# Kernel tuning notes

Measured on AMD Instinct MI355X. Metric: run time of the kernel, lower is better.

## Reference

```python
import jax, jax.numpy as jnp
import numpy as np

N, R, D, T, H, MM, OBJ, PLN = 1024, 100, 256, 14, 8, 600, 36, 16
DH = D // H


def _plin(w, x):
    # monotone piecewise-linear map on [0,1] with PLN segments (Counter's PiecewiseLin)
    w = jnp.abs(w).at[0].set(0.0)
    w = w / w.sum()
    cs = jnp.cumsum(w)  # knot values, cs[PLN] == 1
    y = PLN * jnp.clip(x, 0.0, 1.0)
    i = jnp.clip(jnp.floor(y).astype(jnp.int32), 0, PLN)
    f = y - jnp.floor(y)
    return cs[i] + f * w[jnp.clip(i + 1, 0, PLN)]


def _iou(b):
    # b: (N, m, 4) as x1,y1,x2,y2 -> pairwise IoU (N, m, m)
    area = jnp.clip(b[..., 2] - b[..., 0], 0.0) * jnp.clip(b[..., 3] - b[..., 1], 0.0)
    lt = jnp.maximum(b[:, :, None, :2], b[:, None, :, :2])
    rb = jnp.minimum(b[:, :, None, 2:], b[:, None, :, 2:])
    wh = jnp.clip(rb - lt, 0.0)
    inter = wh[..., 0] * wh[..., 1]
    return inter / (area[:, :, None] + area[:, None, :] - inter + 1e-12)


def _counter(boxes, att, pw):
    # Zhang et al. counting module, already_sigmoided=True
    att_top, idx = jax.lax.top_k(att, OBJ)                       # (N, m)
    btop = jnp.take_along_axis(boxes, idx[:, :, None], axis=1)   # (N, m, 4)
    rel = att_top[:, :, None] * att_top[:, None, :]              # outer product of attention
    dist = 1.0 - _iou(btop)
    score = _plin(pw[0], rel) * _plin(pw[1], dist)
    dscore = _plin(pw[3], rel) * _plin(pw[4], dist)
    # deduplication via outer differences
    att_diff = jnp.abs(att_top[:, :, None] - att_top[:, None, :])
    sd = jnp.abs(dscore[:, :, :, None] - dscore[:, :, None, :])  # (N, m, m, m)
    sim = jnp.prod(_plin(pw[2], 1.0 - sd), axis=1) * _plin(pw[2], 1.0 - att_diff)
    row_sims = sim.sum(axis=2)                                   # (N, m), >= 1 (diagonal)
    all_sims = row_sims[:, :, None] * row_sims[:, None, :]
    score = score / all_sims
    correction = _plin(pw[0], att_top * att_top) / row_sims
    total = jnp.sqrt(score.sum(axis=(1, 2)) + correction.sum(axis=1) + 1e-20)  # (N,)
    # to_one_hot: soft one-hot between floor and ceil counts
    s = jnp.clip(total, 0.0, float(OBJ))
    i = jnp.clip(jnp.floor(s).astype(jnp.int32), 0, OBJ)
    f = s - jnp.floor(s)
    oh_l = jax.nn.one_hot(i, OBJ + 1, dtype=s.dtype)
    oh_r = jax.nn.one_hot(jnp.clip(i + 1, 0, OBJ), OBJ + 1, dtype=s.dtype)
    one_hot = (1.0 - f)[:, None] * oh_l + f[:, None] * oh_r
    att_conf = jnp.abs(_plin(pw[5], att_top) - 0.5)
    dist_conf = jnp.abs(_plin(pw[6], dist) - 0.5)
    conf = _plin(pw[7], att_conf.mean(axis=1) + dist_conf.mean(axis=(1, 2)))  # (N,)
    return one_hot * conf[:, None], conf


def _layernorm(x, g, b):
    mu = x.mean(-1, keepdims=True)
    var = ((x - mu) ** 2).mean(-1, keepdims=True)
    return (x - mu) / jnp.sqrt(var + 1e-5) * g + b


def setup_inputs():
    key = jax.random.key(0)
    ks = jax.random.split(key, 20)
    lin = lambda k, o, i: jax.random.normal(k, (o, i), dtype=jnp.float32) * 0.02
    z = lambda o: jnp.zeros((o,), jnp.float32)
    v_emb = jax.random.normal(ks[0], (N, R, D), dtype=jnp.float32)
    q_emb = jax.random.normal(ks[1], (N, T, D), dtype=jnp.float32)
    xy = jax.random.uniform(ks[2], (N, R, 2), dtype=jnp.float32) * 0.8
    wh = jax.random.uniform(ks[3], (N, R, 2), dtype=jnp.float32) * 0.19 + 0.01
    boxes = jnp.concatenate([xy, xy + wh], axis=-1)  # valid x1,y1,x2,y2 in [0,1]
    pw = jax.random.uniform(ks[4], (8, PLN + 1), dtype=jnp.float32, minval=0.5, maxval=1.5)
    pw = pw.at[:, 0].set(0.0)
    return {
        'v_emb': v_emb, 'q_emb': q_emb, 'boxes': boxes,
        'Wq': lin(ks[5], D, D), 'bq': z(D),
        'Wk': lin(ks[6], D, D), 'bk': z(D),
        'Wv': lin(ks[7], D, D), 'bv': z(D),
        'in_w': lin(ks[8], 3 * D, D), 'in_b': z(3 * D),
        'out_w': lin(ks[9], D, D), 'out_b': z(D),
        'ln_g': jnp.ones((D,), jnp.float32), 'ln_b': z(D),
        'l0_w': lin(ks[10], MM, D), 'l0_b': z(MM),
        'l1_w': lin(ks[11], MM, D), 'l1_b': z(MM),
        'lo_w': lin(ks[12], 1, MM), 'lo_b': z(1),
        'pw': pw,
    }


def reference(v_emb, q_emb, boxes, Wq, bq, Wk, bk, Wv, bv, in_w, in_b, out_w, out_b,
              ln_g, ln_b, l0_w, l0_b, l1_w, l1_b, lo_w, lo_b, pw):
    n = v_emb.shape[0]
    # pre-projections then nn.MultiheadAttention (eval, no dropout)
    q = v_emb @ Wq.T + bq
    k = v_emb @ Wk.T + bk
    v = v_emb @ Wv.T + bv
    wq, wk, wv = jnp.split(in_w, 3, axis=0)
    biq, bik, biv = jnp.split(in_b, 3)
    qh = (q @ wq.T + biq).reshape(n, R, H, DH)
    kh = (k @ wk.T + bik).reshape(n, R, H, DH)
    vh = (v @ wv.T + biv).reshape(n, R, H, DH)
    logits = jnp.einsum('nqhd,nkhd->nhqk', qh, kh) * (1.0 / np.sqrt(DH))
    attn = jax.nn.softmax(logits, axis=-1)
    ao = jnp.einsum('nhqk,nkhd->nqhd', attn, vh).reshape(n, R, D)
    ao = ao @ out_w.T + out_b
    inter = _layernorm(ao, ln_g, ln_b)
    # MLB bilinear fusion with mean-pooled question, normalize=True, no activations
    q_pool = q_emb.mean(axis=1)                 # (N, D)
    x0 = inter @ l0_w.T + l0_b                  # (N, R, MM)
    x1 = q_pool @ l1_w.T + l1_b                 # (N, MM)
    zf = x0 * x1[:, None, :]
    zf = jnp.sign(zf) * jnp.sqrt(jnp.abs(zf))   # signed sqrt
    zf = zf / jnp.maximum(jnp.linalg.norm(zf, axis=-1, keepdims=True), 1e-12)
    scores = jax.nn.sigmoid(zf @ lo_w.T + lo_b)  # (N, R, 1)
    pred, conf = _counter(boxes, scores[..., 0], pw)
    return scores, pred, conf
```

## Files before the change

kernel.cpp:

```cpp
#include <hip/hip_runtime.h>

#define N_   1024
#define R_   100
#define D_   256
#define T_   14
#define H_   8
#define DH_  32
#define MM_  600
#define OBJ_ 36

typedef _Float16 f16;
typedef __attribute__((ext_vector_type(8))) _Float16 f16x8;
typedef __attribute__((ext_vector_type(4))) _Float16 f16x4v;
typedef __attribute__((ext_vector_type(4))) float f32x4;

__device__ __forceinline__ void f2h_split(float x, f16& hi, f16& lo) {
  hi = (_Float16)x;
  lo = (_Float16)(x - (float)hi);
}

#define GL16(gp, lp) __builtin_amdgcn_global_load_lds( \
    (const __attribute__((address_space(1))) void*)(gp), \
    (__attribute__((address_space(3))) void*)(lp), 16, 0, 0)

__device__ __forceinline__ void xcd_remap(int& bx, int& by) {
  int nx = gridDim.x, ny = gridDim.y;
  if ((nx & 7) == 0) {
    int id = bx + nx * by;
    int xcd = id & 7, slot = id >> 3;
    bx = xcd + 8 * (slot / ny);
    by = slot % ny;
  }
}

__device__ __forceinline__ float plin_f(const float* __restrict__ w,
                                        const float* __restrict__ cs, float x) {
  float xc = fminf(fmaxf(x, 0.f), 1.f);
  float y  = 16.f * xc;
  float fy = floorf(y);
  int   i  = (int)fy;
  float f  = y - fy;
  int   ip = i + 1; if (ip > 16) ip = 16;
  return cs[i] + f * w[ip];
}

__global__ void prep_plin(const float* __restrict__ pw, float* __restrict__ plw,
                          float* __restrict__ plc) {
  int p = threadIdx.x;
  if (p < 8) {
    float w[17];
    float sum = 0.f;
    w[0] = 0.f;
    for (int k = 1; k < 17; ++k) { w[k] = fabsf(pw[p*17 + k]); sum += w[k]; }
    float inv = 1.f / sum;
    float c = 0.f;
    for (int k = 0; k < 17; ++k) {
      float wk = w[k] * inv;
      c += wk;
      plw[p*17 + k] = wk;
      plc[p*17 + k] = c;
    }
  }
}

__global__ void fuse_c(const float* __restrict__ in_w, const float* __restrict__ in_b,
                       const float* __restrict__ bq, const float* __restrict__ bk,
                       const float* __restrict__ bv, float* __restrict__ c) {
  int i = blockIdx.x * blockDim.x + threadIdx.x;
  if (i < 768) {
    const float* bsel = (i < 256) ? bq : ((i < 512) ? bk : bv);
    float acc = in_b[i];
    for (int o = 0; o < 256; ++o) acc += in_w[(size_t)i*256 + o] * bsel[o];
    c[i] = acc;
  }
}

__global__ __launch_bounds__(256) void fuse_A(const float* __restrict__ in_w,
    const float* __restrict__ Wq, const float* __restrict__ Wk,
    const float* __restrict__ Wv, f16* __restrict__ Ahi, f16* __restrict__ Alo) {
  int i = blockIdx.x;
  int j = threadIdx.x;
  const float* Wsel = (i < 256) ? Wq : ((i < 512) ? Wk : Wv);
  __shared__ float row[256];
  row[j] = in_w[(size_t)i*256 + j];
  __syncthreads();
  float acc = 0.f;
  for (int o = 0; o < 256; ++o) acc += row[o] * Wsel[(size_t)o*256 + j];
  f16 h, l; f2h_split(acc, h, l);
  Ahi[(size_t)i*256 + j] = h;
  Alo[(size_t)i*256 + j] = l;
}

__global__ __launch_bounds__(256) void split_vec(const float* __restrict__ in,
    f16* __restrict__ hi, f16* __restrict__ lo, int n4) {
  int i = blockIdx.x * blockDim.x + threadIdx.x;
  if (i < n4) {
    float4 v = ((const float4*)in)[i];
    union { f16 h[4]; ushort4 u; } H, L;
    f2h_split(v.x, H.h[0], L.h[0]);
    f2h_split(v.y, H.h[1], L.h[1]);
    f2h_split(v.z, H.h[2], L.h[2]);
    f2h_split(v.w, H.h[3], L.h[3]);
    ((ushort4*)hi)[i] = H.u;
    ((ushort4*)lo)[i] = L.u;
  }
}

__global__ __launch_bounds__(256) void conv_w600(const float* __restrict__ w,
    f16* __restrict__ hi, f16* __restrict__ lo) {
  int o = blockIdx.x;
  int j = threadIdx.x;
  f16 h = (f16)0.f, l = (f16)0.f;
  if (o < 600) f2h_split(w[(size_t)o*256 + j], h, l);
  hi[(size_t)o*256 + j] = h;
  lo[(size_t)o*256 + j] = l;
}

__global__ __launch_bounds__(256) void pool_split(const float* __restrict__ q_emb,
    f16* __restrict__ qph, f16* __restrict__ qpl) {
  int n = blockIdx.x, tid = threadIdx.x;
  float s = 0.f;
  for (int t = 0; t < 14; ++t) s += q_emb[((size_t)n*14 + t)*256 + tid];
  s *= (1.f/14.f);
  f16 h, l; f2h_split(s, h, l);
  qph[(size_t)n*256 + tid] = h;
  qpl[(size_t)n*256 + tid] = l;
}

template<bool BOUND>
__global__ __launch_bounds__(256) void gemm_f16s(
    const f16* __restrict__ Xhi, const f16* __restrict__ Xlo,
    const f16* __restrict__ Whi, const f16* __restrict__ Wlo,
    const float* __restrict__ bias, float* __restrict__ C, int Oreal) {
  __shared__ f16 XsH[128 * 32];
  __shared__ f16 XsL[128 * 32];
  __shared__ f16 WsH[128 * 32];
  __shared__ f16 WsL[128 * 32];
  const int tid  = threadIdx.x;
  const int wave = tid >> 6, lane = tid & 63;
  int bx = blockIdx.x, by = blockIdx.y;
  xcd_remap(bx, by);
  const int bm = bx * 128, bn = by * 128;
  const int wm = (wave & 1) * 64, wn = (wave >> 1) * 64;
  const int col = lane & 15, quad = lane >> 4;

  const int s = wave * 64 + lane;
  const int r0 = s >> 2,         cseg = (s & 3) * 8;
  const int r1 = (s + 256) >> 2;
  const size_t o0 = (size_t)(bm + r0) * 256 + cseg;
  const size_t o1 = (size_t)(bm + r1) * 256 + cseg;
  const size_t p0 = (size_t)(bn + r0) * 256 + cseg;
  const size_t p1 = (size_t)(bn + r1) * 256 + cseg;
  char* XHB = (char*)XsH + wave * 1024;
  char* XLB = (char*)XsL + wave * 1024;
  char* WHB = (char*)WsH + wave * 1024;
  char* WLB = (char*)WsL + wave * 1024;

  f32x4 acc[4][4] = {};

  for (int k0 = 0; k0 < 256; k0 += 32) {
    GL16(Xhi + o0 + k0, XHB);
    GL16(Xhi + o1 + k0, XHB + 4096);
    GL16(Xlo + o0 + k0, XLB);
    GL16(Xlo + o1 + k0, XLB + 4096);
    GL16(Whi + p0 + k0, WHB);
    GL16(Whi + p1 + k0, WHB + 4096);
    GL16(Wlo + p0 + k0, WLB);
    GL16(Wlo + p1 + k0, WLB + 4096);
    __syncthreads();

    f16x8 ah[4], al[4], bh[4], bl[4];
#pragma unroll
    for (int i = 0; i < 4; ++i) {
      int ro = (wm + i*16 + col) * 32 + quad * 8;
      ah[i] = *(const f16x8*)(XsH + ro);
      al[i] = *(const f16x8*)(XsL + ro);
    }
#pragma unroll
    for (int j = 0; j < 4; ++j) {
      int ro = (wn + j*16 + col) * 32 + quad * 8;
      bh[j] = *(const f16x8*)(WsH + ro);
      bl[j] = *(const f16x8*)(WsL + ro);
    }
#pragma unroll
    for (int i = 0; i < 4; ++i)
#pragma unroll
      for (int j = 0; j < 4; ++j) {
        acc[i][j] = __builtin_amdgcn_mfma_f32_16x16x32_f16(al[i], bh[j], acc[i][j], 0, 0, 0);
        acc[i][j] = __builtin_amdgcn_mfma_f32_16x16x32_f16(ah[i], bl[j], acc[i][j], 0, 0, 0);
        acc[i][j] = __builtin_amdgcn_mfma_f32_16x16x32_f16(ah[i], bh[j], acc[i][j], 0, 0, 0);
      }
    __syncthreads();
  }

#pragma unroll
  for (int j = 0; j < 4; ++j) {
    int o = bn + wn + j*16 + col;
    if (BOUND && o >= Oreal) continue;
    float bo = bias[o];
#pragma unroll
    for (int i = 0; i < 4; ++i) {
#pragma unroll
      for (int r = 0; r < 4; ++r) {
        int m = bm + wm + i*16 + quad*4 + r;
        C[(size_t)m * Oreal + o] = acc[i][j][r] + bo;
      }
    }
  }
}

__global__ __launch_bounds__(256) void gemm_l0_mlb(
    const f16* __restrict__ Xhi, const f16* __restrict__ Xlo,
    const f16* __restrict__ Whi, const f16* __restrict__ Wlo,
    const float* __restrict__ bias, const float* __restrict__ x1,
    const float* __restrict__ lo_w, float2* __restrict__ part) {
  __shared__ f16 XsH[128 * 32];
  __shared__ f16 XsL[128 * 32];
  __shared__ f16 WsH[128 * 32];
  __shared__ f16 WsL[128 * 32];
  const int tid  = threadIdx.x;
  const int wave = tid >> 6, lane = tid & 63;
  int bx = blockIdx.x, by = blockIdx.y;
  xcd_remap(bx, by);
  const int bm = bx * 128, bn = by * 128;
  const int wm = (wave & 1) * 64, wn = (wave >> 1) * 64;
  const int col = lane & 15, quad = lane >> 4;

  const int s = wave * 64 + lane;
  const int r0 = s >> 2,         cseg = (s & 3) * 8;
  const int r1 = (s + 256) >> 2;
  const size_t o0 = (size_t)(bm + r0) * 256 + cseg;
  const size_t o1 = (size_t)(bm + r1) * 256 + cseg;
  const size_t p0 = (size_t)(bn + r0) * 256 + cseg;
  const size_t p1 = (size_t)(bn + r1) * 256 + cseg;
  char* XHB = (char*)XsH + wave * 1024;
  char* XLB = (char*)XsL + wave * 1024;
  char* WHB = (char*)WsH + wave * 1024;
  char* WLB = (char*)WsL + wave * 1024;

  f32x4 acc[4][4] = {};

  for (int k0 = 0; k0 < 256; k0 += 32) {
    GL16(Xhi + o0 + k0, XHB);
    GL16(Xhi + o1 + k0, XHB + 4096);
    GL16(Xlo + o0 + k0, XLB);
    GL16(Xlo + o1 + k0, XLB + 4096);
    GL16(Whi + p0 + k0, WHB);
    GL16(Whi + p1 + k0, WHB + 4096);
    GL16(Wlo + p0 + k0, WLB);
    GL16(Wlo + p1 + k0, WLB + 4096);
    __syncthreads();

    f16x8 ah[4], al[4], bh[4], bl[4];
#pragma unroll
    for (int i = 0; i < 4; ++i) {
      int ro = (wm + i*16 + col) * 32 + quad * 8;
      ah[i] = *(const f16x8*)(XsH + ro);
      al[i] = *(const f16x8*)(XsL + ro);
    }
#pragma unroll
    for (int j = 0; j < 4; ++j) {
      int ro = (wn + j*16 + col) * 32 + quad * 8;
      bh[j] = *(const f16x8*)(WsH + ro);
      bl[j] = *(const f16x8*)(WsL + ro);
    }
#pragma unroll
    for (int i = 0; i < 4; ++i)
#pragma unroll
      for (int j = 0; j < 4; ++j) {
        acc[i][j] = __builtin_amdgcn_mfma_f32_16x16x32_f16(al[i], bh[j], acc[i][j], 0, 0, 0);
        acc[i][j] = __builtin_amdgcn_mfma_f32_16x16x32_f16(ah[i], bl[j], acc[i][j], 0, 0, 0);
        acc[i][j] = __builtin_amdgcn_mfma_f32_16x16x32_f16(ah[i], bh[j], acc[i][j], 0, 0, 0);
      }
    __syncthreads();
  }

  const int M = (int)gridDim.x * 128;
  const int NCimg = M / 100;
  const int mA = bm + wm;
  const int imgA = mA / 100;
  int imgB = imgA + 1; if (imgB > NCimg - 1) imgB = NCimg - 1;
  const int rB = (imgA + 1) * 100;

  float bo4[4], lw4[4], x1A[4], x1B[4];
#pragma unroll
  for (int j = 0; j < 4; ++j) {
    int o = bn + wn + j*16 + col;
    bool v = (o < 600);
    bo4[j] = v ? bias[o] : 0.f;
    lw4[j] = v ? lo_w[o] : 0.f;
    x1A[j] = v ? x1[(size_t)imgA*600 + o] : 0.f;
    x1B[j] = v ? x1[(size_t)imgB*600 + o] : 0.f;
  }

#pragma unroll
  for (int i = 0; i < 4; ++i) {
#pragma unroll
    for (int rr = 0; rr < 4; ++rr) {
      int m = bm + wm + i*16 + quad*4 + rr;
      bool hiImg = (m >= rB);
      float ss = 0.f, dt = 0.f;
#pragma unroll
      for (int j = 0; j < 4; ++j) {
        float xv = hiImg ? x1B[j] : x1A[j];
        float v = (acc[i][j][rr] + bo4[j]) * xv;
        float av = fabsf(v);
        ss += av;
        dt += copysignf(sqrtf(av), v) * lw4[j];
      }
#pragma unroll
      for (int msk = 1; msk < 16; msk <<= 1) {
        ss += __shfl_xor(ss, msk, 64);
        dt += __shfl_xor(dt, msk, 64);
      }
      if (col == 0) {
        float2 pv; pv.x = ss; pv.y = dt;
        part[(size_t)m * 10 + by * 2 + (wn >> 6)] = pv;
      }
    }
  }
}

__global__ __launch_bounds__(256) void mlb_reduce(const float2* __restrict__ part,
    const float* __restrict__ lo_b, float* __restrict__ out, int M) {
  int m = blockIdx.x * 256 + threadIdx.x;
  if (m < M) {
    const float2* p = part + (size_t)m * 10;
    float ss = 0.f, dt = 0.f;
#pragma unroll
    for (int t = 0; t < 10; ++t) { float2 v = p[t]; ss += v.x; dt += v.y; }
    float sc = dt / fmaxf(sqrtf(ss), 1e-12f) + lo_b[0];
    out[m] = 1.f / (1.f + __expf(-sc));
  }
}

__global__ __launch_bounds__(256) void gemm2_ln(
    const f16* __restrict__ Xhi, const f16* __restrict__ Xlo,
    const f16* __restrict__ Whi, const f16* __restrict__ Wlo,
    const float* __restrict__ bias, const float* __restrict__ g,
    const float* __restrict__ b, f16* __restrict__ ohi, f16* __restrict__ olo) {
  __shared__ f16 XsH[128 * 32];
  __shared__ f16 XsL[128 * 32];
  __shared__ f16 WsH[256 * 32];
  __shared__ f16 WsL[256 * 32];
  __shared__ float gbb[768];
  const int tid  = threadIdx.x;
  const int wave = tid >> 6, lane = tid & 63;
  const int bm = blockIdx.x * 128;
  const int wm = wave * 32;
  const int col16 = lane & 15, quad = lane >> 4;

  for (int i = tid; i < 768; i += 256)
    gbb[i] = (i < 256) ? g[i] : ((i < 512) ? b[i - 256] : bias[i - 512]);

  const int s = wave * 64 + lane;
  const int rx0 = s >> 2, cseg = (s & 3) * 8;
  const int rx1 = (s + 256) >> 2;
  const size_t o0 = (size_t)(bm + rx0) * 256 + cseg;
  const size_t o1 = (size_t)(bm + rx1) * 256 + cseg;
  char* XHB = (char*)XsH + wave * 1024;
  char* XLB = (char*)XsL + wave * 1024;

  f32x4 acc[2][16] = {};

  for (int k0 = 0; k0 < 256; k0 += 32) {
    GL16(Xhi + o0 + k0, XHB);
    GL16(Xhi + o1 + k0, XHB + 4096);
    GL16(Xlo + o0 + k0, XLB);
    GL16(Xlo + o1 + k0, XLB + 4096);
#pragma unroll
    for (int is = 0; is < 4; ++is) {
      int sw = is * 256 + s;
      size_t wo = (size_t)(sw >> 2) * 256 + (sw & 3) * 8 + k0;
      GL16(Whi + wo, (char*)WsH + is * 4096 + wave * 1024);
      GL16(Wlo + wo, (char*)WsL + is * 4096 + wave * 1024);
    }
    __syncthreads();

    f16x8 ah[2], al[2];
#pragma unroll
    for (int i = 0; i < 2; ++i) {
      int ro = (wm + i*16 + col16) * 32 + quad * 8;
      ah[i] = *(const f16x8*)(XsH + ro);
      al[i] = *(const f16x8*)(XsL + ro);
    }
#pragma unroll
    for (int j = 0; j < 16; ++j) {
      int ro = (j*16 + col16) * 32 + quad * 8;
      f16x8 bh = *(const f16x8*)(WsH + ro);
      f16x8 bl = *(const f16x8*)(WsL + ro);
#pragma unroll
      for (int i = 0; i < 2; ++i) {
        acc[i][j] = __builtin_amdgcn_mfma_f32_16x16x32_f16(al[i], bh, acc[i][j], 0, 0, 0);
        acc[i][j] = __builtin_amdgcn_mfma_f32_16x16x32_f16(ah[i], bl, acc[i][j], 0, 0, 0);
        acc[i][j] = __builtin_amdgcn_mfma_f32_16x16x32_f16(ah[i], bh, acc[i][j], 0, 0, 0);
      }
    }
    __syncthreads();
  }

#pragma unroll
  for (int i = 0; i < 2; ++i) {
#pragma unroll
    for (int r = 0; r < 4; ++r) {
      float x[16];
      float sum = 0.f;
#pragma unroll
      for (int j = 0; j < 16; ++j) {
        float v = acc[i][j][r] + gbb[512 + j*16 + col16];
        x[j] = v;
        sum += v;
      }
#pragma unroll
      for (int msk = 1; msk < 16; msk <<= 1) sum += __shfl_xor(sum, msk, 64);
      float mu = sum * (1.f/256.f);
      float s2 = 0.f;
#pragma unroll
      for (int j = 0; j < 16; ++j) { float d = x[j] - mu; s2 += d * d; }
#pragma unroll
      for (int msk = 1; msk < 16; msk <<= 1) s2 += __shfl_xor(s2, msk, 64);
      float inv = rsqrtf(s2 * (1.f/256.f) + 1e-5f);
      size_t m = (size_t)(bm + wm + i*16 + quad*4 + r);
#pragma unroll
      for (int j = 0; j < 16; ++j) {
        int col = j*16 + col16;
        float yv = (x[j] - mu) * inv * gbb[col] + gbb[256 + col];
        f16 hh, ll; f2h_split(yv, hh, ll);
        ohi[m*256 + col] = hh;
        olo[m*256 + col] = ll;
      }
    }
  }
}

__global__ __launch_bounds__(512) void attn_mfma(const float* __restrict__ qkv,
    f16* __restrict__ aohi, f16* __restrict__ aolo) {
  const int n = blockIdx.x >> 3;
  const int h = blockIdx.x & 7;
  __shared__ f16 KH[112*32], KL[112*32];
  __shared__ f16 VTH[32*116], VTL[32*116];
  __shared__ unsigned int P32[112*116];
  const int tid = threadIdx.x;
  const int wave = tid >> 6, lane = tid & 63;
  const int col16 = lane & 15, quad = lane >> 4;
  const float scale = 0.17677669529663687f;
  const float* base = qkv + (size_t)n * 100 * 768 + h * 32;
  const int tm = wave;

  float qv[8];
  if (tm < 7) {
    int m = tm*16 + col16; if (m > 99) m = 99;
    const float* qp = base + (size_t)m * 768 + quad*8;
    float4 q0 = *(const float4*)(qp);
    float4 q1 = *(const float4*)(qp + 4);
    qv[0]=q0.x; qv[1]=q0.y; qv[2]=q0.z; qv[3]=q0.w;
    qv[4]=q1.x; qv[5]=q1.y; qv[6]=q1.z; qv[7]=q1.w;
  } else {
#pragma unroll
    for (int j = 0; j < 8; ++j) qv[j] = 0.f;
  }

  for (int idx = tid; idx < 112*32; idx += 512) {
    int r = idx >> 5, d = idx & 31;
    float kv = 0.f, vv = 0.f;
    if (r < 100) {
      const float* p = base + (size_t)r * 768;
      kv = p[256 + d];
      vv = p[512 + d];
    }
    f16 khh, kll, vhh, vll;
    f2h_split(kv, khh, kll);
    f2h_split(vv, vhh, vll);
    KH[idx] = khh; KL[idx] = kll;
    VTH[d*116 + r] = vhh; VTL[d*116 + r] = vll;
  }
  __syncthreads();

  if (tm < 7) {
    f16x8 ah, al;
#pragma unroll
    for (int j = 0; j < 8; ++j) {
      f16 hh, ll; f2h_split(qv[j] * scale, hh, ll); ah[j] = hh; al[j] = ll;
    }
    f32x4 sacc[7];
#pragma unroll
    for (int tn = 0; tn < 7; ++tn) {
      int off = (tn*16 + col16)*32 + quad*8;
      f16x8 bh = *(const f16x8*)(KH + off);
      f16x8 bl = *(const f16x8*)(KL + off);
      f32x4 a = {};
      a = __builtin_amdgcn_mfma_f32_16x16x32_f16(al, bh, a, 0, 0, 0);
      a = __builtin_amdgcn_mfma_f32_16x16x32_f16(ah, bl, a, 0, 0, 0);
      a = __builtin_amdgcn_mfma_f32_16x16x32_f16(ah, bh, a, 0, 0, 0);
      sacc[tn] = a;
    }
    if (col16 >= 4) {
      sacc[6][0] = -1e30f; sacc[6][1] = -1e30f;
      sacc[6][2] = -1e30f; sacc[6][3] = -1e30f;
    }
    float mx[4];
#pragma unroll
    for (int r = 0; r < 4; ++r) {
      float mv = sacc[0][r];
#pragma unroll
      for (int tn = 1; tn < 7; ++tn) mv = fmaxf(mv, sacc[tn][r]);
      mx[r] = mv;
    }
#pragma unroll
    for (int msk = 1; msk < 16; msk <<= 1)
#pragma unroll
      for (int r = 0; r < 4; ++r) mx[r] = fmaxf(mx[r], __shfl_xor(mx[r], msk, 64));
    float sm[4] = {0.f, 0.f, 0.f, 0.f};
#pragma unroll
    for (int tn = 0; tn < 7; ++tn)
#pragma unroll
      for (int r = 0; r < 4; ++r) {
        float p = __expf(sacc[tn][r] - mx[r]);
        sacc[tn][r] = p;
        sm[r] += p;
      }
#pragma unroll
    for (int msk = 1; msk < 16; msk <<= 1)
#pragma unroll
      for (int r = 0; r < 4; ++r) sm[r] += __shfl_xor(sm[r], msk, 64);
    float inv[4];
#pragma unroll
    for (int r = 0; r < 4; ++r) inv[r] = 1.f / sm[r];
#pragma unroll
    for (int tn = 0; tn < 7; ++tn)
#pragma unroll
      for (int r = 0; r < 4; ++r) {
        float p = sacc[tn][r] * inv[r];
        f16 hh, ll; f2h_split(p, hh, ll);
        union { struct { f16 h, l; } f; unsigned int u; } pk;
        pk.f.h = hh; pk.f.l = ll;
        P32[(tm*16 + quad*4 + r)*116 + tn*16 + col16] = pk.u;
      }

    f16x8 vh[2][4], vl[2][4];
#pragma unroll
    for (int td = 0; td < 2; ++td)
#pragma unroll
      for (int kc = 0; kc < 4; ++kc) {
        if (kc == 3 && quad >= 2) {
          f16x8 z = {};
          vh[td][kc] = z; vl[td][kc] = z;
        } else {
          int off = (td*16 + col16)*116 + kc*32 + quad*8;
          f16x4v h0 = *(const f16x4v*)(VTH + off);
          f16x4v h1 = *(const f16x4v*)(VTH + off + 4);
          f16x4v l0 = *(const f16x4v*)(VTL + off);
          f16x4v l1 = *(const f16x4v*)(VTL + off + 4);
          f16x8 hv, lv;
#pragma unroll
          for (int t = 0; t < 4; ++t) { hv[t] = h0[t]; hv[t+4] = h1[t]; lv[t] = l0[t]; lv[t+4] = l1[t]; }
          vh[td][kc] = hv; vl[td][kc] = lv;
        }
      }
    f32x4 acc[2] = {};
#pragma unroll
    for (int kc = 0; kc < 4; ++kc) {
      f16x8 ph, pl;
      if (kc == 3 && quad >= 2) {
        f16x8 z = {};
        ph = z; pl = z;
      } else {
        const unsigned int* pp = P32 + (tm*16 + col16)*116 + kc*32 + quad*8;
        f16x8 e0 = *(const f16x8*)(pp);
        f16x8 e1 = *(const f16x8*)(pp + 4);
        ph = __builtin_shufflevector(e0, e1, 0, 2, 4, 6, 8, 10, 12, 14);
        pl = __builtin_shufflevector(e0, e1, 1, 3, 5, 7, 9, 11, 13, 15);
      }
#pragma unroll
      for (int td = 0; td < 2; ++td) {
        acc[td] = __builtin_amdgcn_mfma_f32_16x16x32_f16(pl, vh[td][kc], acc[td], 0, 0, 0);
        acc[td] = __builtin_amdgcn_mfma_f32_16x16x32_f16(ph, vl[td][kc], acc[td], 0, 0, 0);
        acc[td] = __builtin_amdgcn_mfma_f32_16x16x32_f16(ph, vh[td][kc], acc[td], 0, 0, 0);
      }
    }
#pragma unroll
    for (int td = 0; td < 2; ++td) {
#pragma unroll
      for (int r = 0; r < 4; ++r) {
        int m = tm*16 + quad*4 + r;
        if (m < 100) {
          size_t oidx = ((size_t)n*100 + m)*256 + h*32 + td*16 + col16;
          f16 hh, ll; f2h_split(acc[td][r], hh, ll);
          aohi[oidx] = hh;
          aolo[oidx] = ll;
        }
      }
    }
  }
}

__device__ __forceinline__ float breduce(float v, float* red, int tid) {
  for (int o = 32; o > 0; o >>= 1) v += __shfl_down(v, o, 64);
  if ((tid & 63) == 0) red[tid >> 6] = v;
  __syncthreads();
  float r = red[0] + red[1] + red[2] + red[3];
  __syncthreads();
  return r;
}

__global__ __launch_bounds__(256) void counter_kernel(
    const float* __restrict__ scores, const float* __restrict__ boxes,
    const float* __restrict__ plw, const float* __restrict__ plc,
    float* __restrict__ pred, float* __restrict__ conf_out) {
  int n = blockIdx.x, tid = threadIdx.x;
  __shared__ float plw_s[8][17], plc_s[8][17];
  __shared__ float sval[128];
  __shared__ int   sidx[128];
  __shared__ float att[36], bx[36][4];
  __shared__ float dist[36][36], scr[36][36], ds2[36][36], sim[36][36];
  __shared__ float rs[36];
  __shared__ float red[4];
  __shared__ float b_f, b_cf;
  __shared__ int   b_i;

  for (int i = tid; i < 136; i += 256) {
    (&plw_s[0][0])[i] = plw[i];
    (&plc_s[0][0])[i] = plc[i];
  }
  if (tid < 128) {
    sval[tid] = (tid < 100) ? scores[(size_t)n*100 + tid] : -1e30f;
    sidx[tid] = tid;
  }
  __syncthreads();

  for (int k = 2; k <= 128; k <<= 1) {
    for (int j = k >> 1; j > 0; j >>= 1) {
      if (tid < 128) {
        int ixj = tid ^ j;
        if (ixj > tid) {
          float va = sval[tid], vb = sval[ixj];
          int   ia = sidx[tid], ib = sidx[ixj];
          bool a_before_b = (va > vb) || (va == vb && ia < ib);
          bool ascending = ((tid & k) == 0);
          bool doswap = ascending ? !a_before_b : a_before_b;
          if (doswap) { sval[tid] = vb; sval[ixj] = va; sidx[tid] = ib; sidx[ixj] = ia; }
        }
      }
      __syncthreads();
    }
  }

  if (tid < 36) {
    att[tid] = sval[tid];
    const float* bp = boxes + ((size_t)n*100 + sidx[tid])*4;
    bx[tid][0] = bp[0]; bx[tid][1] = bp[1]; bx[tid][2] = bp[2]; bx[tid][3] = bp[3];
  }
  __syncthreads();

  for (int idx = tid; idx < 1296; idx += 256) {
    int i = idx / 36, j = idx % 36;
    float x1a = bx[i][0], y1a = bx[i][1], x2a = bx[i][2], y2a = bx[i][3];
    float x1b = bx[j][0], y1b = bx[j][1], x2b = bx[j][2], y2b = bx[j][3];
    float areaA = fmaxf(x2a - x1a, 0.f) * fmaxf(y2a - y1a, 0.f);
    float areaB = fmaxf(x2b - x1b, 0.f) * fmaxf(y2b - y1b, 0.f);
    float iw = fmaxf(fminf(x2a, x2b) - fmaxf(x1a, x1b), 0.f);
    float ih = fmaxf(fminf(y2a, y2b) - fmaxf(y1a, y1b), 0.f);
    float inter = iw * ih;
    float iou = inter / (areaA + areaB - inter + 1e-12f);
    float dd = 1.f - iou;
    float rel = att[i] * att[j];
    dist[i][j] = dd;
    scr[i][j]  = plin_f(plw_s[0], plc_s[0], rel) * plin_f(plw_s[1], plc_s[1], dd);
    ds2[i][j]  = plin_f(plw_s[3], plc_s[3], rel) * plin_f(plw_s[4], plc_s[4], dd);
  }
  __syncthreads();

  for (int idx = tid; idx < 1296; idx += 256) {
    int b = idx / 36, c = idx % 36;
    float p = plin_f(plw_s[2], plc_s[2], 1.f - fabsf(att[b] - att[c]));
    for (int a = 0; a < 36; ++a)
      p *= plin_f(plw_s[2], plc_s[2], 1.f - fabsf(ds2[a][b] - ds2[a][c]));
    sim[b][c] = p;
  }
  __syncthreads();

  if (tid < 36) {
    float s = 0.f;
    for (int c = 0; c < 36; ++c) s += sim[tid][c];
    rs[tid] = s;
  }
  __syncthreads();

  float p1 = 0.f, p4 = 0.f;
  for (int idx = tid; idx < 1296; idx += 256) {
    int b = idx / 36, c = idx % 36;
    p1 += scr[b][c] / (rs[b] * rs[c]);
    p4 += fabsf(plin_f(plw_s[6], plc_s[6], dist[b][c]) - 0.5f);
  }
  float p2 = 0.f, p3 = 0.f;
  if (tid < 36) {
    p2 = plin_f(plw_s[0], plc_s[0], att[tid]*att[tid]) / rs[tid];
    p3 = fabsf(plin_f(plw_s[5], plc_s[5], att[tid]) - 0.5f);
  }
  float s1 = breduce(p1, red, tid);
  float s2 = breduce(p2, red, tid);
  float s3 = breduce(p3, red, tid);
  float s4 = breduce(p4, red, tid);

  if (tid == 0) {
    float total = sqrtf(s1 + s2 + 1e-20f);
    float cf = plin_f(plw_s[7], plc_s[7], s3 * (1.f/36.f) + s4 * (1.f/1296.f));
    float sc = fminf(fmaxf(total, 0.f), 36.f);
    float fl = floorf(sc);
    int ii = (int)fl; if (ii > 36) ii = 36;
    b_f = sc - fl;
    b_i = ii;
    b_cf = cf;
    conf_out[n] = cf;
  }
  __syncthreads();
  if (tid < 37) {
    int ii = b_i;
    int ir = (ii + 1 > 36) ? 36 : ii + 1;
    float v = ((tid == ii) ? (1.f - b_f) : 0.f) + ((tid == ir) ? b_f : 0.f);
    pred[(size_t)n*37 + tid] = v * b_cf;
  }
}

extern "C" void kernel_launch(void* const* d_in, const int* in_sizes, int n_in,
                              void* d_out, int out_size, void* d_ws, size_t ws_size,
                              hipStream_t stream) {
  const float* v_emb = (const float*)d_in[0];
  const float* q_emb = (const float*)d_in[1];
  const float* boxes = (const float*)d_in[2];
  const float* Wq    = (const float*)d_in[3];
  const float* bq    = (const float*)d_in[4];
  const float* Wk    = (const float*)d_in[5];
  const float* bk    = (const float*)d_in[6];
  const float* Wv    = (const float*)d_in[7];
  const float* bv    = (const float*)d_in[8];
  const float* in_w  = (const float*)d_in[9];
  const float* in_b  = (const float*)d_in[10];
  const float* out_w = (const float*)d_in[11];
  const float* out_b = (const float*)d_in[12];
  const float* ln_g  = (const float*)d_in[13];
  const float* ln_b  = (const float*)d_in[14];
  const float* l0_w  = (const float*)d_in[15];
  const float* l0_b  = (const float*)d_in[16];
  const float* l1_w  = (const float*)d_in[17];
  const float* l1_b  = (const float*)d_in[18];
  const float* lo_w  = (const float*)d_in[19];
  const float* lo_b  = (const float*)d_in[20];
  const float* pw    = (const float*)d_in[21];

  float* ws = (float*)d_ws;
  float* plw   = ws + 0;
  float* plc   = ws + 256;
  float* cbuf  = ws + 512;
  float* x1    = ws + 1280;
  f16* hb = (f16*)(ws + 615680);
  f16* A_hi    = hb + 0;
  f16* A_lo    = hb + 196608;
  f16* outw_hi = hb + 393216;
  f16* outw_lo = hb + 458752;
  f16* l0w_hi  = hb + 524288;
  f16* l0w_lo  = hb + 688128;
  f16* l1w_hi  = hb + 851968;
  f16* l1w_lo  = hb + 1015808;
  f16* qp_hi   = hb + 1179648;
  f16* qp_lo   = hb + 1441792;
  f16* v_hi    = hb + 1703936;
  f16* v_lo    = hb + 27918336;
  const size_t small_floats = 615680 + 27066368;

  size_t avail = (ws_size / 4 > small_floats) ? (ws_size / 4 - small_floats) : 0;
  int NC = 1024;
  while (NC > 32 && (size_t)NC * 130000ull > avail) NC >>= 1;

  float* qkv_c = ws + small_floats;
  float2* part = (float2*)(qkv_c + (size_t)NC * 76800);
  f16* ao_hi  = (f16*)((float*)(void*)part + (size_t)NC * 2000);
  f16* ao_lo  = ao_hi + (size_t)NC * 25600;
  f16* int_hi = ao_lo + (size_t)NC * 25600;
  f16* int_lo = int_hi + (size_t)NC * 25600;

  float* out    = (float*)d_out;
  float* scores = out;
  float* pred   = out + 102400;
  float* conf   = out + 140288;

  prep_plin<<<1, 64, 0, stream>>>(pw, plw, plc);
  fuse_c<<<3, 256, 0, stream>>>(in_w, in_b, bq, bk, bv, cbuf);
  fuse_A<<<768, 256, 0, stream>>>(in_w, Wq, Wk, Wv, A_hi, A_lo);
  split_vec<<<(65536/4 + 255)/256, 256, 0, stream>>>(out_w, outw_hi, outw_lo, 65536/4);
  conv_w600<<<640, 256, 0, stream>>>(l0_w, l0w_hi, l0w_lo);
  conv_w600<<<640, 256, 0, stream>>>(l1_w, l1w_hi, l1w_lo);
  split_vec<<<(26214400/4 + 255)/256, 256, 0, stream>>>(v_emb, v_hi, v_lo, 26214400/4);
  pool_split<<<N_, 256, 0, stream>>>(q_emb, qp_hi, qp_lo);
  {
    dim3 gx(1024/128, 5);
    gemm_f16s<true><<<gx, 256, 0, stream>>>(qp_hi, qp_lo, l1w_hi, l1w_lo,
                                            l1_b, x1, 600);
  }

  for (int n0 = 0; n0 < N_; n0 += NC) {
    const int M = NC * 100;
    const size_t voff = (size_t)n0 * 100 * 256;

    dim3 g1(M / 128, 6);
    gemm_f16s<false><<<g1, 256, 0, stream>>>(v_hi + voff, v_lo + voff,
                                             A_hi, A_lo, cbuf, qkv_c, 768);

    attn_mfma<<<NC * H_, 512, 0, stream>>>(qkv_c, ao_hi, ao_lo);

    gemm2_ln<<<M / 128, 256, 0, stream>>>(ao_hi, ao_lo, outw_hi, outw_lo,
                                          out_b, ln_g, ln_b, int_hi, int_lo);

    dim3 g3(M / 128, 5);
    gemm_l0_mlb<<<g3, 256, 0, stream>>>(int_hi, int_lo, l0w_hi, l0w_lo,
                                        l0_b, x1 + (size_t)n0 * 600, lo_w, part);

    mlb_reduce<<<(M + 255)/256, 256, 0, stream>>>(part, lo_b,
                                                  scores + (size_t)n0 * 100, M);
  }

  counter_kernel<<<N_, 256, 0, stream>>>(scores, boxes, plw, plc, pred, conf);
}
```

Before: 882.0 us.

## Fuse QKV projection GEMM into per-head attention kernel

Removes the separate QKV GEMM and its fp32 intermediate buffer. Each attention block now computes its own head's Q, K and V projections from the split-f16 v_emb and the fused weight matrix, staging tiles into LDS with global_load_lds. The results go straight into the K/V LDS layouts and a swizzled Q buffer. This saves the large fp32 qkv write and read-back and allows bigger chunks (NC), at the cost of per-block GEMM work with low reuse. Blocks are also reordered so heads of the same sample land on different positions in the grid.

Result: faster. 809.3 us (-8.2%).

```diff
diff --git a/kernel.cpp b/kernel.cpp
--- a/kernel.cpp
+++ b/kernel.cpp
@@ -433,55 +433,112 @@
   }
 }
 
-__global__ __launch_bounds__(512) void attn_mfma(const float* __restrict__ qkv,
+__global__ __launch_bounds__(512, 4) void attn_fused(
+    const f16* __restrict__ v_hi, const f16* __restrict__ v_lo,
+    const f16* __restrict__ A_hi, const f16* __restrict__ A_lo,
+    const float* __restrict__ cbuf,
     f16* __restrict__ aohi, f16* __restrict__ aolo) {
-  const int n = blockIdx.x >> 3;
-  const int h = blockIdx.x & 7;
+  int b = blockIdx.x;
+  const int nper = (int)(gridDim.x >> 6);
+  const int n = (b & 7) * nper + (b >> 6);
+  const int h = (b >> 3) & 7;
+
   __shared__ f16 KH[112*32], KL[112*32];
   __shared__ f16 VTH[32*116], VTL[32*116];
   __shared__ unsigned int P32[112*116];
+  char* STG = (char*)P32;
+  f16* XsH = (f16*)STG;
+  f16* XsL = XsH + 3584;
+  f16* WsH = XsH + 7168;
+  f16* WsL = XsH + 10240;
+  unsigned int* qsc32 = (unsigned int*)(STG + 37632);
+
   const int tid = threadIdx.x;
   const int wave = tid >> 6, lane = tid & 63;
   const int col16 = lane & 15, quad = lane >> 4;
   const float scale = 0.17677669529663687f;
-  const float* base = qkv + (size_t)n * 100 * 768 + h * 32;
   const int tm = wave;
 
-  float qv[8];
+  float bo[6];
+#pragma unroll
+  for (int j = 0; j < 6; ++j) {
+    int ol = j*16 + col16;
+    bo[j] = cbuf[(ol >> 5)*256 + h*32 + (ol & 31)];
+  }
+
+  f32x4 acc[6] = {};
+  for (int k0 = 0; k0 < 256; k0 += 32) {
+#pragma unroll
+    for (int jj = 0; jj < 4; ++jj) {
+      int c = tid + jj*512;
+      if (c >= 1664) break;
+      const f16* src;
+      if (c < 896) {
+        int cc = (c < 448) ? c : c - 448;
+        int r = cc >> 2; if (r > 99) r = 99;
+        const f16* vb = (c < 448) ? v_hi : v_lo;
+        src = vb + ((size_t)n*100 + r)*256 + k0 + (cc & 3)*8;
+      } else {
+        int cc = (c < 1280) ? c - 896 : c - 1280;
+        int row = cc >> 2;
+        int o = ((row >> 5) << 8) + h*32 + (row & 31);
+        const f16* ab = (c < 1280) ? A_hi : A_lo;
+        src = ab + (size_t)o*256 + k0 + (cc & 3)*8;
+      }
+      GL16(src, STG + (size_t)(c - lane)*16);
+    }
+    __syncthreads();
+    if (tm < 7) {
+      int ro = (tm*16 + col16)*32 + quad*8;
+      f16x8 ah = *(const f16x8*)(XsH + ro);
+      f16x8 al = *(const f16x8*)(XsL + ro);
+#pragma unroll
+      for (int j = 0; j < 6; ++j) {
+        int wo = (j*16 + col16)*32 + quad*8;
+        f16x8 bh = *(const f16x8*)(WsH + wo);
+        f16x8 bl = *(const f16x8*)(WsL + wo);
+        acc[j] = __builtin_amdgcn_mfma_f32_16x16x32_f16(al, bh, acc[j], 0, 0, 0);
+        acc[j] = __builtin_amdgcn_mfma_f32_16x16x32_f16(ah, bl, acc[j], 0, 0, 0);
+        acc[j] = __builtin_amdgcn_mfma_f32_16x16x32_f16(ah, bh, acc[j], 0, 0, 0);
+      }
+    }
+    __syncthreads();
+  }
+
   if (tm < 7) {
-    int m = tm*16 + col16; if (m > 99) m = 99;
-    const float* qp = base + (size_t)m * 768 + quad*8;
-    float4 q0 = *(const float4*)(qp);
-    float4 q1 = *(const float4*)(qp + 4);
-    qv[0]=q0.x; qv[1]=q0.y; qv[2]=q0.z; qv[3]=q0.w;
-    qv[4]=q1.x; qv[5]=q1.y; qv[6]=q1.z; qv[7]=q1.w;
-  } else {
-#pragma unroll
-    for (int j = 0; j < 8; ++j) qv[j] = 0.f;
-  }
-
-  for (int idx = tid; idx < 112*32; idx += 512) {
-    int r = idx >> 5, d = idx & 31;
-    float kv = 0.f, vv = 0.f;
-    if (r < 100) {
-      const float* p = base + (size_t)r * 768;
-      kv = p[256 + d];
-      vv = p[512 + d];
-    }
-    f16 khh, kll, vhh, vll;
-    f2h_split(kv, khh, kll);
-    f2h_split(vv, vhh, vll);
-    KH[idx] = khh; KL[idx] = kll;
-    VTH[d*116 + r] = vhh; VTL[d*116 + r] = vll;
-  }
-  __syncthreads();
-
+#pragma unroll
+    for (int j = 0; j < 2; ++j) {
+#pragma unroll
+      for (int r = 0; r < 4; ++r) {
+        int key = tm*16 + quad*4 + r;
+        int d = j*16 + col16;
+        f16 hh, ll;
+        f2h_split(acc[2+j][r] + bo[2+j], hh, ll);
+        KH[key*32 + d] = hh; KL[key*32 + d] = ll;
+        f2h_split(acc[4+j][r] + bo[4+j], hh, ll);
+        VTH[d*116 + key] = hh; VTL[d*116 + key] = ll;
+        f2h_split((acc[j][r] + bo[j]) * scale, hh, ll);
+        union { struct { f16 h, l; } f; unsigned int u; } pk;
+        pk.f.h = hh; pk.f.l = ll;
+        int mrow = quad*4 + r;
+        qsc32[wave*512 + mrow*32 + (d ^ (r << 3))] = pk.u;
+      }
+    }
+  }
+  __syncthreads();
+
+  f16x8 ah = {}, al = {};
   if (tm < 7) {
-    f16x8 ah, al;
-#pragma unroll
-    for (int j = 0; j < 8; ++j) {
-      f16 hh, ll; f2h_split(qv[j] * scale, hh, ll); ah[j] = hh; al[j] = ll;
-    }
+    int sw = (col16 & 3) << 3;
+    const unsigned int* qp = qsc32 + wave*512 + col16*32 + ((quad*8) ^ sw);
+    f16x8 e0 = *(const f16x8*)(qp);
+    f16x8 e1 = *(const f16x8*)(qp + 4);
+    ah = __builtin_shufflevector(e0, e1, 0, 2, 4, 6, 8, 10, 12, 14);
+    al = __builtin_shufflevector(e0, e1, 1, 3, 5, 7, 9, 11, 13, 15);
+  }
+  __syncthreads();
+
+  if (tm < 7) {
     f32x4 sacc[7];
 #pragma unroll
     for (int tn = 0; tn < 7; ++tn) {
@@ -557,7 +614,7 @@
           vh[td][kc] = hv; vl[td][kc] = lv;
         }
       }
-    f32x4 acc[2] = {};
+    f32x4 oacc[2] = {};
 #pragma unroll
     for (int kc = 0; kc < 4; ++kc) {
       f16x8 ph, pl;
@@ -573,9 +630,9 @@
       }
 #pragma unroll
       for (int td = 0; td < 2; ++td) {
-        acc[td] = __builtin_amdgcn_mfma_f32_16x16x32_f16(pl, vh[td][kc], acc[td], 0, 0, 0);
-        acc[td] = __builtin_amdgcn_mfma_f32_16x16x32_f16(ph, vl[td][kc], acc[td], 0, 0, 0);
-        acc[td] = __builtin_amdgcn_mfma_f32_16x16x32_f16(ph, vh[td][kc], acc[td], 0, 0, 0);
+        oacc[td] = __builtin_amdgcn_mfma_f32_16x16x32_f16(pl, vh[td][kc], oacc[td], 0, 0, 0);
+        oacc[td] = __builtin_amdgcn_mfma_f32_16x16x32_f16(ph, vl[td][kc], oacc[td], 0, 0, 0);
+        oacc[td] = __builtin_amdgcn_mfma_f32_16x16x32_f16(ph, vh[td][kc], oacc[td], 0, 0, 0);
       }
     }
 #pragma unroll
@@ -585,7 +642,7 @@
         int m = tm*16 + quad*4 + r;
         if (m < 100) {
           size_t oidx = ((size_t)n*100 + m)*256 + h*32 + td*16 + col16;
-          f16 hh, ll; f2h_split(acc[td][r], hh, ll);
+          f16 hh, ll; f2h_split(oacc[td][r], hh, ll);
           aohi[oidx] = hh;
           aolo[oidx] = ll;
         }
@@ -770,10 +827,9 @@
 
   size_t avail = (ws_size / 4 > small_floats) ? (ws_size / 4 - small_floats) : 0;
   int NC = 1024;
-  while (NC > 32 && (size_t)NC * 130000ull > avail) NC >>= 1;
-
-  float* qkv_c = ws + small_floats;
-  float2* part = (float2*)(qkv_c + (size_t)NC * 76800);
+  while (NC > 32 && (size_t)NC * 53200ull > avail) NC >>= 1;
+
+  float2* part = (float2*)(ws + small_floats);
   f16* ao_hi  = (f16*)((float*)(void*)part + (size_t)NC * 2000);
   f16* ao_lo  = ao_hi + (size_t)NC * 25600;
   f16* int_hi = ao_lo + (size_t)NC * 25600;
@@ -802,11 +858,8 @@
     const int M = NC * 100;
     const size_t voff = (size_t)n0 * 100 * 256;
 
-    dim3 g1(M / 128, 6);
-    gemm_f16s<false><<<g1, 256, 0, stream>>>(v_hi + voff, v_lo + voff,
-                                             A_hi, A_lo, cbuf, qkv_c, 768);
-
-    attn_mfma<<<NC * H_, 512, 0, stream>>>(qkv_c, ao_hi, ao_lo);
+    attn_fused<<<NC * H_, 512, 0, stream>>>(v_hi + voff, v_lo + voff,
+                                            A_hi, A_lo, cbuf, ao_hi, ao_lo);
 
     gemm2_ln<<<M / 128, 256, 0, stream>>>(ao_hi, ao_lo, outw_hi, outw_lo,
                                           out_b, ln_g, ln_b, int_hi, int_lo);
```
